# Performance work log

Measured on AMD Instinct MI355X. Metric: run time of the kernel, lower is better.

The kernel has to match this reference:

```python
import jax, jax.numpy as jnp
import numpy as np

B, D, H, O = 4096, 1024, 8192, 1000

def setup_inputs() -> dict:
    key = jax.random.key(0)
    k1, k2, k3 = jax.random.split(key, 3)
    x = jax.random.normal(k1, (B, D), dtype=jnp.float32)
    kohonen_weights = jax.random.normal(k2, (H, D), dtype=jnp.float32) * (6.0 / (H + D)) ** 0.5
    grossberg_weights = jax.random.normal(k3, (O, H), dtype=jnp.float32) * (6.0 / (O + H)) ** 0.5
    return {"x": x, "kohonen_weights": kohonen_weights, "grossberg_weights": grossberg_weights}

def reference(x, kohonen_weights, grossberg_weights):
    # but kept faithful since distances only feed argmin -> same winners either way)
    x_sq = jnp.sum(x * x, axis=1, keepdims=True)                      # [B,1]
    w_sq = jnp.sum(kohonen_weights * kohonen_weights, axis=1)         # [H]
    sq_dists = x_sq - 2.0 * (x @ kohonen_weights.T) + w_sq[None, :]   # [B,H]
    winners = jnp.argmin(sq_dists, axis=1)                            # [B]
    # one_hot @ grossberg.T is mathematically a row gather of grossberg.T
    output = grossberg_weights.T[winners]                             # [B,O]
    return output, winners
```

## Files before the change

kernel.cpp:

```cpp
#include <hip/hip_runtime.h>
#include <hip/hip_bf16.h>

#define B_ 4096
#define D_ 1024
#define H_ 8192
#define O_ 1000
#define K2 2048
#define NT 48

typedef __attribute__((ext_vector_type(8))) short short8;
typedef __attribute__((ext_vector_type(4))) short short4v;
typedef __attribute__((ext_vector_type(16))) float f32x16;

union BF4 { __hip_bfloat16 b[4]; short4v s; };

__device__ __forceinline__ void gload16(void* ldsp, const void* g) {
  __builtin_amdgcn_global_load_lds(
      (const __attribute__((address_space(1))) unsigned int*)g,
      (__attribute__((address_space(3))) unsigned int*)ldsp, 16, 0, 0);
}

__device__ __forceinline__ int aoff_(int T) {
  const int t = T / 3, r = T - 3 * t;
  return (r == 1 ? 1024 : 0) + t * 64;
}
__device__ __forceinline__ int boff_(int T) {
  const int t = T / 3, r = T - 3 * t;
  return (r == 2 ? 1024 : 0) + t * 64;
}

__global__ __launch_bounds__(256) void split_all_kernel(
    const float* __restrict__ x, const float* __restrict__ w,
    __hip_bfloat16* __restrict__ Ap, __hip_bfloat16* __restrict__ Bp,
    float* __restrict__ xsq, float* __restrict__ wsq,
    unsigned long long* __restrict__ keys)
{
  const int r = blockIdx.x;
  const int t = threadIdx.x;
  const float* src;
  __hip_bfloat16* dst;
  float* sq;
  if (r < B_) {
    src = x + (size_t)r * D_; dst = Ap + (size_t)r * K2; sq = xsq + r;
    if (t == 0) keys[r] = ~0ULL;
  } else {
    const int rr = r - B_;
    src = w + (size_t)rr * D_; dst = Bp + (size_t)rr * K2; sq = wsq + rr;
  }
  const float4 v = ((const float4*)src)[t];
  float ss = v.x * v.x + v.y * v.y + v.z * v.z + v.w * v.w;

  BF4 Hh, Ll;
  const float e[4] = {v.x, v.y, v.z, v.w};
#pragma unroll
  for (int i = 0; i < 4; ++i) {
    __hip_bfloat16 h = __float2bfloat16(e[i]);
    Hh.b[i] = h;
    Ll.b[i] = __float2bfloat16(e[i] - __bfloat162float(h));
  }
  *(short4v*)(dst + t * 4) = Hh.s;
  *(short4v*)(dst + 1024 + t * 4) = Ll.s;

#pragma unroll
  for (int o = 32; o > 0; o >>= 1) ss += __shfl_down(ss, o);
  __shared__ float wsum[4];
  if ((t & 63) == 0) wsum[t >> 6] = ss;
  __syncthreads();
  if (t == 0) *sq = (wsum[0] + wsum[1]) + (wsum[2] + wsum[3]);
}


#define BAR() do { asm volatile("" ::: "memory"); \
                   __builtin_amdgcn_s_barrier(); \
                   asm volatile("" ::: "memory"); } while (0)
#define SB0() __builtin_amdgcn_sched_barrier(0)
#define GATEV0() asm volatile("s_waitcnt vmcnt(0)")
#define LGKM6() do { asm volatile("s_waitcnt lgkmcnt(6)"); SB0(); } while (0)
#define LGKM0() do { asm volatile("s_waitcnt lgkmcnt(0)"); SB0(); } while (0)

#define DSR(dst, base, OFF) \
  asm volatile("ds_read_b128 %0, %1 offset:" OFF : "=v"(dst) : "v"(base))

#define RDP(F, DSEL, KK) do { \
    const unsigned a_ = aB + (DSEL) + ofk##KK; \
    const unsigned b_ = bB + (DSEL) + ofk##KK; \
    DSR(F[0], a_, "0");    DSR(F[1], a_, "4096"); \
    DSR(F[2], a_, "8192"); DSR(F[3], a_, "12288"); \
    DSR(F[4], b_, "0");    DSR(F[5], b_, "4096"); \
  } while (0)

#define STAGE(P, prow, T, isB, h) do { if ((T) < NT) { \
    const int koff_ = (isB) ? boff_(T) : aoff_(T); \
    const __hip_bfloat16* s0_ = (P) + (size_t)((prow) + (h)*128 + wid*16 + srow) * K2 + koff_ + sunit0 * 8; \
    const __hip_bfloat16* s1_ = (P) + (size_t)((prow) + (h)*128 + wid*16 + 8 + srow) * K2 + koff_ + sunit1 * 8; \
    char* d_ = lds + ((T)&1)*65536 + (isB)*32768 + (h)*16384 + wid*2048 + lane*16; \
    gload16(d_, s0_); gload16(d_ + 1024, s1_); } } while (0)

#define MFMA32(a, b, c) __builtin_amdgcn_mfma_f32_32x32x16_bf16(a, b, c, 0, 0, 0)

#define MMQ32(F) do { \
    __builtin_amdgcn_s_setprio(1); \
    acc[0][0] = MFMA32(F[0], F[4], acc[0][0]); \
    acc[0][1] = MFMA32(F[0], F[5], acc[0][1]); \
    acc[1][0] = MFMA32(F[1], F[4], acc[1][0]); \
    acc[1][1] = MFMA32(F[1], F[5], acc[1][1]); \
    acc[2][0] = MFMA32(F[2], F[4], acc[2][0]); \
    acc[2][1] = MFMA32(F[2], F[5], acc[2][1]); \
    acc[3][0] = MFMA32(F[3], F[4], acc[3][0]); \
    acc[3][1] = MFMA32(F[3], F[5], acc[3][1]); \
    __builtin_amdgcn_s_setprio(0); \
    SB0(); } while (0)

#define TILE32(DSEL, T) do { \
    GATEV0(); BAR(); \
    RDP(f0, DSEL, 0); \
    RDP(f1, DSEL, 1); \
    STAGE(Ap, brow, (T) + 1, 0, 0); \
    STAGE(Bp, bcol, (T) + 1, 1, 0); \
    LGKM6(); MMQ32(f0); \
    RDP(f0, DSEL, 2); \
    STAGE(Ap, brow, (T) + 1, 0, 1); \
    STAGE(Bp, bcol, (T) + 1, 1, 1); \
    LGKM6(); MMQ32(f1); \
    RDP(f1, DSEL, 3); \
    LGKM6(); MMQ32(f0); \
    LGKM0(); MMQ32(f1); \
  } while (0)

__global__ __launch_bounds__(512, 2) void gemm_argmin_kernel(
    const __hip_bfloat16* __restrict__ Ap, const __hip_bfloat16* __restrict__ Bp,
    const float* __restrict__ xsq, const float* __restrict__ wsq,
    unsigned long long* __restrict__ keys)
{
  __shared__ char lds[131072];

  const int t = threadIdx.x;
  const int id = blockIdx.x;
  const int xcd = id & 7;
  const int r_ = id >> 3;
  const int by = (xcd >> 2) * 8 + (r_ >> 3);
  const int bx = (xcd & 3) * 8 + (r_ & 7);
  const int brow = by * 256, bcol = bx * 256;

  const int lane = t & 63, wid = t >> 6;
  const int wm = wid >> 2, wn = wid & 3;
  const int c31 = lane & 31;
  const int kh = lane >> 5;
  const int swz = lane & 7;
  const int hi2 = (c31 >> 3) & 3;
  const unsigned fsw = (unsigned)(swz ^ hi2);

  const unsigned ofk0 = (((0u + kh) ^ fsw) * 16);
  const unsigned ofk1 = (((2u + kh) ^ fsw) * 16);
  const unsigned ofk2 = (((4u + kh) ^ fsw) * 16);
  const unsigned ofk3 = (((6u + kh) ^ fsw) * 16);

  const unsigned lb = (unsigned)(uintptr_t)lds;
  const unsigned aB = lb + (unsigned)(wm * 16384 + c31 * 128);
  const unsigned bB = lb + (unsigned)(32768 + (wn >> 1) * 16384 +
                                      ((wn & 1) * 64 + c31) * 128);

  const int srow = lane >> 3;
  const int sunit0 = (lane & 7) ^ srow ^ ((2 * wid) & 3);
  const int sunit1 = (lane & 7) ^ srow ^ ((2 * wid + 1) & 3);

  f32x16 acc[4][2] = {};
  short8 f0[6], f1[6];

  STAGE(Ap, brow, 0, 0, 0);
  STAGE(Ap, brow, 0, 0, 1);
  STAGE(Bp, bcol, 0, 1, 0);
  STAGE(Bp, bcol, 0, 1, 1);

  for (int tt = 0; tt < NT; tt += 2) {
    TILE32(0, tt);
    TILE32(65536, tt + 1);
  }

#pragma unroll
  for (int m = 0; m < 4; ++m) {
#pragma unroll
    for (int rg = 0; rg < 16; ++rg) {
      const int row = brow + wm * 128 + m * 32 + (rg & 3) + 8 * (rg >> 2) + 4 * kh;
      const float xs = xsq[row];
      unsigned long long best = ~0ULL;
#pragma unroll
      for (int n = 0; n < 2; ++n) {
        const int col = bcol + wn * 64 + n * 32 + c31;
        const float s = (xs - 2.0f * acc[m][n][rg]) + wsq[col];
        unsigned ub = __float_as_uint(s);
        ub = (ub & 0x80000000u) ? ~ub : (ub | 0x80000000u);
        const unsigned long long key =
            ((unsigned long long)ub << 32) | (unsigned)col;
        if (key < best) best = key;
      }
#pragma unroll
      for (int o = 1; o < 32; o <<= 1) {
        const unsigned long long v = __shfl_xor(best, o);
        if (v < best) best = v;
      }
      if (c31 == 0) atomicMin(&keys[row], best);
    }
  }
}

__global__ __launch_bounds__(256) void transposeG_kernel(
    const float* __restrict__ G, float* __restrict__ GT)
{
  __shared__ float tile[32][33];
  const int h0 = blockIdx.x * 32;
  const int o0 = blockIdx.y * 32;
  const int tx = threadIdx.x;
  const int ty = threadIdx.y;
#pragma unroll
  for (int j = 0; j < 4; ++j) {
    const int o = o0 + ty + j * 8;
    if (o < O_) tile[ty + j * 8][tx] = G[(size_t)o * H_ + h0 + tx];
  }
  __syncthreads();
  const int o = o0 + tx;
  if (o < O_) {
#pragma unroll
    for (int j = 0; j < 4; ++j)
      GT[(size_t)(h0 + ty + j * 8) * O_ + o] = tile[tx][ty + j * 8];
  }
}

__global__ __launch_bounds__(256) void finalize_kernel(
    const unsigned long long* __restrict__ keys,
    const float* __restrict__ GT, float* __restrict__ out)
{
  const int b = blockIdx.x;
  const unsigned w = (unsigned)(keys[b] & 0xFFFFFFFFull);
  if (threadIdx.x == 0) out[(size_t)B_ * O_ + b] = (float)w;
  const float4* src = (const float4*)(GT + (size_t)w * O_);
  float4* dst = (float4*)(out + (size_t)b * O_);
  for (int i = threadIdx.x; i < O_ / 4; i += 256) dst[i] = src[i];
}

extern "C" void kernel_launch(void* const* d_in, const int* in_sizes, int n_in,
                              void* d_out, int out_size, void* d_ws, size_t ws_size,
                              hipStream_t stream)
{
  (void)in_sizes; (void)n_in; (void)out_size; (void)ws_size;
  const float* x = (const float*)d_in[0];
  const float* kw = (const float*)d_in[1];
  const float* gw = (const float*)d_in[2];
  float* out = (float*)d_out;

  char* ws = (char*)d_ws;
  __hip_bfloat16* Ap = (__hip_bfloat16*)(ws);
  __hip_bfloat16* Bp = (__hip_bfloat16*)(ws + 16777216);
  float* xsq = (float*)(ws + 50331648);
  float* wsq = (float*)(ws + 50331648 + 16384);
  unsigned long long* keys = (unsigned long long*)(ws + 50331648 + 16384 + 32768);
  float* GT = (float*)(ws);

  split_all_kernel<<<B_ + H_, 256, 0, stream>>>(x, kw, Ap, Bp, xsq, wsq, keys);
  gemm_argmin_kernel<<<512, 512, 0, stream>>>(Ap, Bp, xsq, wsq, keys);
  transposeG_kernel<<<dim3(H_ / 32, (O_ + 31) / 32), dim3(32, 8), 0, stream>>>(gw, GT);
  finalize_kernel<<<B_, 256, 0, stream>>>(keys, GT, out);
}
```

Measured before the change: 288.6 us.

## Switch GEMM mainloop to 4-stage LDS ring with half-depth K tiles

```diff
diff --git a/kernel.cpp b/kernel.cpp
--- a/kernel.cpp
+++ b/kernel.cpp
@@ -6,7 +6,7 @@
 #define H_ 8192
 #define O_ 1000
 #define K2 2048
-#define NT 48
+#define NT 96
 
 typedef __attribute__((ext_vector_type(8))) short short8;
 typedef __attribute__((ext_vector_type(4))) short short4v;
@@ -20,13 +20,13 @@
       (__attribute__((address_space(3))) unsigned int*)ldsp, 16, 0, 0);
 }
 
-__device__ __forceinline__ int aoff_(int T) {
-  const int t = T / 3, r = T - 3 * t;
-  return (r == 1 ? 1024 : 0) + t * 64;
-}
-__device__ __forceinline__ int boff_(int T) {
-  const int t = T / 3, r = T - 3 * t;
-  return (r == 2 ? 1024 : 0) + t * 64;
+__device__ __forceinline__ int aoff32_(int T) {
+  const int g = T >> 1, t = g / 3, r = g - 3 * t;
+  return (r == 1 ? 1024 : 0) + t * 64 + (T & 1) * 32;
+}
+__device__ __forceinline__ int boff32_(int T) {
+  const int g = T >> 1, t = g / 3, r = g - 3 * t;
+  return (r == 2 ? 1024 : 0) + t * 64 + (T & 1) * 32;
 }
 
 __global__ __launch_bounds__(256) void split_all_kernel(
@@ -74,7 +74,7 @@
                    __builtin_amdgcn_s_barrier(); \
                    asm volatile("" ::: "memory"); } while (0)
 #define SB0() __builtin_amdgcn_sched_barrier(0)
-#define GATEV0() asm volatile("s_waitcnt vmcnt(0)")
+#define GATE_S(S) asm volatile("s_waitcnt vmcnt(" S ")" ::: "memory")
 #define LGKM6() do { asm volatile("s_waitcnt lgkmcnt(6)"); SB0(); } while (0)
 #define LGKM0() do { asm volatile("s_waitcnt lgkmcnt(0)"); SB0(); } while (0)
 
@@ -84,17 +84,21 @@
 #define RDP(F, DSEL, KK) do { \
     const unsigned a_ = aB + (DSEL) + ofk##KK; \
     const unsigned b_ = bB + (DSEL) + ofk##KK; \
-    DSR(F[0], a_, "0");    DSR(F[1], a_, "4096"); \
-    DSR(F[2], a_, "8192"); DSR(F[3], a_, "12288"); \
-    DSR(F[4], b_, "0");    DSR(F[5], b_, "4096"); \
+    DSR(F[0], a_, "0");    DSR(F[1], a_, "2048"); \
+    DSR(F[2], a_, "4096"); DSR(F[3], a_, "6144"); \
+    DSR(F[4], b_, "0");    DSR(F[5], b_, "2048"); \
   } while (0)
 
-#define STAGE(P, prow, T, isB, h) do { if ((T) < NT) { \
-    const int koff_ = (isB) ? boff_(T) : aoff_(T); \
-    const __hip_bfloat16* s0_ = (P) + (size_t)((prow) + (h)*128 + wid*16 + srow) * K2 + koff_ + sunit0 * 8; \
-    const __hip_bfloat16* s1_ = (P) + (size_t)((prow) + (h)*128 + wid*16 + 8 + srow) * K2 + koff_ + sunit1 * 8; \
-    char* d_ = lds + ((T)&1)*65536 + (isB)*32768 + (h)*16384 + wid*2048 + lane*16; \
-    gload16(d_, s0_); gload16(d_ + 1024, s1_); } } while (0)
+#define STAGE_A(T) do { \
+    const int ka_ = aoff32_(T); \
+    char* d_ = lds + ((T)&3)*32768 + wid*2048 + lane*16; \
+    gload16(d_,        gA0 + ka_); \
+    gload16(d_ + 1024, gA1 + ka_); } while (0)
+#define STAGE_B(T) do { \
+    const int kb_ = boff32_(T); \
+    char* d_ = lds + ((T)&3)*32768 + 16384 + wid*2048 + lane*16; \
+    gload16(d_,        gB0 + kb_); \
+    gload16(d_ + 1024, gB1 + kb_); } while (0)
 
 #define MFMA32(a, b, c) __builtin_amdgcn_mfma_f32_32x32x16_bf16(a, b, c, 0, 0, 0)
 
@@ -111,20 +115,18 @@
     __builtin_amdgcn_s_setprio(0); \
     SB0(); } while (0)
 
-#define TILE32(DSEL, T) do { \
-    GATEV0(); BAR(); \
-    RDP(f0, DSEL, 0); \
+#define TILE(DSEL, D1SEL, T, DOSTAGE, GS, DONEXT) do { \
+     \
     RDP(f1, DSEL, 1); \
-    STAGE(Ap, brow, (T) + 1, 0, 0); \
-    STAGE(Bp, bcol, (T) + 1, 1, 0); \
-    LGKM6(); MMQ32(f0); \
-    RDP(f0, DSEL, 2); \
-    STAGE(Ap, brow, (T) + 1, 0, 1); \
-    STAGE(Bp, bcol, (T) + 1, 1, 1); \
-    LGKM6(); MMQ32(f1); \
-    RDP(f1, DSEL, 3); \
-    LGKM6(); MMQ32(f0); \
-    LGKM0(); MMQ32(f1); \
+    if (DOSTAGE) STAGE_A((T) + 3); \
+    LGKM6(); \
+    MMQ32(f0); \
+     \
+    if (DONEXT) RDP(f0, D1SEL, 0); \
+    if (DOSTAGE) STAGE_B((T) + 3); \
+    if (DONEXT) { LGKM6(); } else { LGKM0(); } \
+    MMQ32(f1); \
+    GATE_S(GS); BAR(); \
   } while (0)
 
 __global__ __launch_bounds__(512, 2) void gemm_argmin_kernel(
@@ -146,36 +148,44 @@
   const int wm = wid >> 2, wn = wid & 3;
   const int c31 = lane & 31;
   const int kh = lane >> 5;
-  const int swz = lane & 7;
-  const int hi2 = (c31 >> 3) & 3;
-  const unsigned fsw = (unsigned)(swz ^ hi2);
+  const unsigned fsw = (unsigned)((c31 >> 3) & 3);
 
   const unsigned ofk0 = (((0u + kh) ^ fsw) * 16);
   const unsigned ofk1 = (((2u + kh) ^ fsw) * 16);
-  const unsigned ofk2 = (((4u + kh) ^ fsw) * 16);
-  const unsigned ofk3 = (((6u + kh) ^ fsw) * 16);
 
   const unsigned lb = (unsigned)(uintptr_t)lds;
-  const unsigned aB = lb + (unsigned)(wm * 16384 + c31 * 128);
-  const unsigned bB = lb + (unsigned)(32768 + (wn >> 1) * 16384 +
-                                      ((wn & 1) * 64 + c31) * 128);
-
-  const int srow = lane >> 3;
-  const int sunit0 = (lane & 7) ^ srow ^ ((2 * wid) & 3);
-  const int sunit1 = (lane & 7) ^ srow ^ ((2 * wid + 1) & 3);
+  const unsigned aB = lb + (unsigned)(wm * 8192 + c31 * 64);
+  const unsigned bB = lb + (unsigned)(16384 + wn * 4096 + c31 * 64);
+
+  const int sr = lane >> 2;
+  const int su0 = (lane & 3) ^ (lane >> 5);
+  const int su1 = su0 ^ 2;
+  const __hip_bfloat16* gA0 = Ap + (size_t)(brow + wid * 32 + sr) * K2 + su0 * 8;
+  const __hip_bfloat16* gA1 = Ap + (size_t)(brow + wid * 32 + 16 + sr) * K2 + su1 * 8;
+  const __hip_bfloat16* gB0 = Bp + (size_t)(bcol + wid * 32 + sr) * K2 + su0 * 8;
+  const __hip_bfloat16* gB1 = Bp + (size_t)(bcol + wid * 32 + 16 + sr) * K2 + su1 * 8;
 
   f32x16 acc[4][2] = {};
   short8 f0[6], f1[6];
 
-  STAGE(Ap, brow, 0, 0, 0);
-  STAGE(Ap, brow, 0, 0, 1);
-  STAGE(Bp, bcol, 0, 1, 0);
-  STAGE(Bp, bcol, 0, 1, 1);
-
-  for (int tt = 0; tt < NT; tt += 2) {
-    TILE32(0, tt);
-    TILE32(65536, tt + 1);
-  }
+  STAGE_A(0); STAGE_B(0);
+  STAGE_A(1); STAGE_B(1);
+  STAGE_A(2); STAGE_B(2);
+  GATE_S("4");
+  BAR();
+  RDP(f0, 0, 0);
+  SB0();
+
+  for (int tb = 0; tb < NT - 4; tb += 4) {
+    TILE(0,     32768, tb + 0, 1, "4", 1);
+    TILE(32768, 65536, tb + 1, 1, "4", 1);
+    TILE(65536, 98304, tb + 2, 1, "4", 1);
+    TILE(98304, 0,     tb + 3, 1, "4", 1);
+  }
+  TILE(0,     32768, NT - 4, 1, "4", 1);
+  TILE(32768, 65536, NT - 3, 0, "0", 1);
+  TILE(65536, 98304, NT - 2, 0, "0", 1);
+  TILE(98304, 0,     NT - 1, 0, "0", 0);
 
 #pragma unroll
   for (int m = 0; m < 4; ++m) {
```

Measured after the change: 291.7 us. No clear change (+1.1%).
